# Kernel tuning notes

Hardware: AMD Instinct MI355X
Metric: run time of the kernel (lower is better)

The kernel has to match this reference:

```python
import jax, jax.numpy as jnp
import numpy as np

N_CYCLES = 20000  # number of cycles in the cycle basis (segments)


def setup_inputs() -> dict:
    key = jax.random.key(0)
    k1, k2, k3, k4, k5 = jax.random.split(key, 5)
    B, NB, E = 256, 50000, 160000  # batch, n_branches, total cycle-basis entries
    c = jax.random.normal(k1, (B, NB), dtype=jnp.float32)
    s = jax.random.normal(k2, (B, NB), dtype=jnp.float32)
    # signs are +/-1
    cysigns = jnp.where(jax.random.uniform(k4, (E,)) < 0.5, -1.0, 1.0).astype(jnp.float32)
    cyinds = jax.random.randint(k3, (E,), 0, NB, dtype=jnp.int32)
    # from_value_rowids requires nondecreasing row ids
    cyrows = jnp.sort(jax.random.randint(k5, (E,), 0, N_CYCLES, dtype=jnp.int32))
    return {"c": c, "s": s, "cysigns": cysigns, "cyinds": cyinds, "cyrows": cyrows}


def reference(c, s, cysigns, cyinds, cyrows):
    # gather branch vars per cycle-basis entry: [B, E]
    cg = jnp.take(c, cyinds, axis=1)
    sg = cysigns * jnp.take(s, cyinds, axis=1)
    # tf.math.angle(tf.complex(rc, rs)) == atan2(imag, real)
    ang = jnp.arctan2(sg, cg)  # [B, E]
    # ragged per-cycle sum == segment_sum over the entry axis -> [N_CYCLES, B]
    v_kvl = jax.ops.segment_sum(ang.T, cyrows, num_segments=N_CYCLES)
    # scalar KVL violation
    return jnp.mean(jnp.abs(v_kvl))
```

## Files before the change

kernel.cpp:

```cpp
#include <hip/hip_runtime.h>

#define NB     50000
#define NB4    12500
#define BATCH  256
#define NCYC   20000
#define QSCALE  (127.0f / 3.14159265358979f)
#define DQSCALE (3.14159265358979f / 127.0f)
#define OUTSCALE (1.0f / ((float)NCYC * (float)BATCH))

__device__ __forceinline__ float fast_atan2q(float y, float x) {
    const float ax = __builtin_fabsf(x);
    const float ay = __builtin_fabsf(y);
    const float mx = fmaxf(ax, ay);
    const float mn = fminf(ax, ay);
    const float t  = mn * __builtin_amdgcn_rcpf(mx);
    const float t2 = t * t;
    float p = fmaf(t2, fmaf(t2, fmaf(t2, fmaf(t2,
                  0.84219761f, -3.44137383f), 7.28200966f), -13.35163894f),
                  40.42416382f);
    p *= t;
    p = (ay > ax) ? (63.5f - p) : p;
    p = (x < 0.0f) ? (127.0f - p) : p;
    return copysignf(p, y);
}

__device__ __forceinline__ unsigned int q8(float y, float x) {
    return (unsigned int)(unsigned char)(signed char)__float2int_rn(fast_atan2q(y, x));
}

__device__ __forceinline__ void gload16(const void* g, void* l) {
    __builtin_amdgcn_global_load_lds(
        (const __attribute__((address_space(1))) void*)g,
        (__attribute__((address_space(3))) void*)l,
        16, 0, 0);
}

__global__ __launch_bounds__(256) void theta_k(
        const float4* __restrict__ c4, const float4* __restrict__ s4,
        signed char* __restrict__ th, int* __restrict__ row_start,
        const int* __restrict__ rows, int E) {
    __shared__ float4 ct[16][64];
    __shared__ float4 st[16][64];
    const int u = threadIdx.x;

    if (blockIdx.y == 0) {
        const int g = blockIdx.x * 256 + u;
        if (g <= NCYC) {
            int lo = 0, hi = E;
            while (lo < hi) { const int m = (lo + hi) >> 1; if (rows[m] < g) lo = m + 1; else hi = m; }
            row_start[g] = lo;
        }
    }

    const int lane  = u & 63;
    const int w     = u >> 6;
    const int brow0 = blockIdx.y * 16;
    int col = blockIdx.x * 64 + lane;
    if (col > NB4 - 1) col = NB4 - 1;

    #pragma unroll
    for (int i = 0; i < 4; ++i) {
        const int r = 4 * w + i;
        gload16(&c4[(size_t)(brow0 + r) * NB4 + col], &ct[r][0]);
        gload16(&s4[(size_t)(brow0 + r) * NB4 + col], &st[r][0]);
    }
    __syncthreads();

    const float* cf = reinterpret_cast<const float*>(ct);
    const float* sf = reinterpret_cast<const float*>(st);
    unsigned int wv[4] = {0u, 0u, 0u, 0u};
    #pragma unroll
    for (int r = 0; r < 16; ++r) {
        const float cc = cf[r * 256 + u];
        const float ss = sf[r * 256 + u];
        wv[r >> 2] |= q8(ss, cc) << (8 * (r & 3));
    }

    const int nbg = blockIdx.x * 256 + u;
    if (nbg < NB) {
        uint4 o;
        o.x = wv[0]; o.y = wv[1]; o.z = wv[2]; o.w = wv[3];
        *reinterpret_cast<uint4*>(&th[(size_t)nbg * BATCH + brow0]) = o;
    }
}

__global__ __launch_bounds__(256) void kvl3_k(
        const signed char* __restrict__ th,
        const float* __restrict__ signs, const int* __restrict__ inds,
        const int* __restrict__ row_start,
        float* __restrict__ partials) {
    __shared__ float wsum[4];
    const int tid  = threadIdx.x;
    const int wave = tid >> 6;
    const int lane = tid & 63;
    const int r    = blockIdx.x * 4 + wave;
    const int start = row_start[r];
    const int end   = row_start[r + 1];

    float a0 = 0.f, a1 = 0.f, a2 = 0.f, a3 = 0.f;
    int e = start;
    for (; e + 2 <= end; e += 2) {
        const int   i0 = inds[e],  i1 = inds[e + 1];
        const float g0 = signs[e] * DQSCALE, g1 = signs[e + 1] * DQSCALE;
        const unsigned int u0 = *reinterpret_cast<const unsigned int*>(&th[(size_t)i0 * BATCH + lane * 4]);
        const unsigned int u1 = *reinterpret_cast<const unsigned int*>(&th[(size_t)i1 * BATCH + lane * 4]);
        a0 += g0 * (float)(signed char)(u0      ) + g1 * (float)(signed char)(u1      );
        a1 += g0 * (float)(signed char)(u0 >>  8) + g1 * (float)(signed char)(u1 >>  8);
        a2 += g0 * (float)(signed char)(u0 >> 16) + g1 * (float)(signed char)(u1 >> 16);
        a3 += g0 * (float)(signed char)(u0 >> 24) + g1 * (float)(signed char)(u1 >> 24);
    }
    if (e < end) {
        const float g0 = signs[e] * DQSCALE;
        const unsigned int u0 = *reinterpret_cast<const unsigned int*>(&th[(size_t)inds[e] * BATCH + lane * 4]);
        a0 += g0 * (float)(signed char)(u0      );
        a1 += g0 * (float)(signed char)(u0 >>  8);
        a2 += g0 * (float)(signed char)(u0 >> 16);
        a3 += g0 * (float)(signed char)(u0 >> 24);
    }
    float v = fabsf(a0) + fabsf(a1) + fabsf(a2) + fabsf(a3);
    #pragma unroll
    for (int off = 32; off > 0; off >>= 1)
        v += __shfl_down(v, off, 64);
    if (lane == 0) wsum[wave] = v;
    __syncthreads();
    if (tid == 0)
        partials[blockIdx.x] = wsum[0] + wsum[1] + wsum[2] + wsum[3];
}

__global__ __launch_bounds__(1024) void reduce_k(
        const float* __restrict__ partials, float* __restrict__ out) {
    const int tid = threadIdx.x;
    float v = 0.f;
    for (int i = tid; i < NCYC / 4; i += 1024) v += partials[i];
    #pragma unroll
    for (int off = 32; off > 0; off >>= 1)
        v += __shfl_down(v, off, 64);
    __shared__ float wsum[16];
    if ((tid & 63) == 0) wsum[tid >> 6] = v;
    __syncthreads();
    if (tid == 0) {
        float t = 0.f;
        #pragma unroll
        for (int w = 0; w < 16; ++w) t += wsum[w];
        out[0] = t * OUTSCALE;
    }
}

__global__ void zero_out_k(float* out) { if (threadIdx.x == 0) out[0] = 0.0f; }

__global__ __launch_bounds__(256) void kvl_fallback_k(
        const float* __restrict__ c, const float* __restrict__ s,
        const float* __restrict__ signs, const int* __restrict__ inds,
        const int* __restrict__ rows, int E, float* __restrict__ out) {
    const int r = blockIdx.x;
    int lo = 0, hi = E;
    while (lo < hi) { const int m = (lo + hi) >> 1; if (rows[m] < r) lo = m + 1; else hi = m; }
    const int start = lo;
    hi = E;
    while (lo < hi) { const int m = (lo + hi) >> 1; if (rows[m] <= r) lo = m + 1; else hi = m; }
    const int end = lo;
    const int tid = threadIdx.x;
    float acc = 0.f;
    for (int e = start; e < end; ++e) {
        const int idx = inds[e];
        const float sg = signs[e];
        acc += atan2f(sg * s[(size_t)tid * NB + idx], c[(size_t)tid * NB + idx]);
    }
    float v = fabsf(acc);
    #pragma unroll
    for (int off = 32; off > 0; off >>= 1)
        v += __shfl_down(v, off, 64);
    __shared__ float wsum[4];
    if ((tid & 63) == 0) wsum[tid >> 6] = v;
    __syncthreads();
    if (tid == 0)
        atomicAdd(out, (wsum[0] + wsum[1] + wsum[2] + wsum[3]) *
                       (1.0f / ((float)NCYC * (float)BATCH)));
}

extern "C" void kernel_launch(void* const* d_in, const int* in_sizes, int n_in,
                              void* d_out, int out_size, void* d_ws, size_t ws_size,
                              hipStream_t stream) {
    const float* c       = (const float*)d_in[0];
    const float* s       = (const float*)d_in[1];
    const float* cysigns = (const float*)d_in[2];
    const int*   cyinds  = (const int*)d_in[3];
    const int*   cyrows  = (const int*)d_in[4];
    const int    E       = in_sizes[2];
    float* out = (float*)d_out;

    const size_t th_bytes = (size_t)NB * BATCH;
    const size_t rs_bytes = (size_t)(NCYC + 1) * sizeof(int);
    const size_t pa_bytes = (size_t)(NCYC / 4) * sizeof(float);
    const size_t need = th_bytes + rs_bytes + pa_bytes;
    if (ws_size >= need) {
        signed char* th   = (signed char*)d_ws;
        int* row_start    = (int*)(th + th_bytes);
        float* partials   = (float*)((char*)row_start + rs_bytes);

        dim3 tg((NB4 + 63) / 64, 16);
        theta_k<<<tg, 256, 0, stream>>>((const float4*)c, (const float4*)s,
                                        th, row_start, cyrows, E);
        kvl3_k<<<NCYC / 4, 256, 0, stream>>>(th, cysigns, cyinds, row_start,
                                             partials);
        reduce_k<<<1, 1024, 0, stream>>>(partials, out);
    } else {
        zero_out_k<<<1, 64, 0, stream>>>(out);
        kvl_fallback_k<<<NCYC, 256, 0, stream>>>(c, s, cysigns, cyinds, cyrows, E, out);
    }
}
```

Before: 152.7 us.

## Double-buffer per-wave theta tiles and unroll the KVL gather loop by four

theta_k now gives each wave its own 256-branch by 16-batch unit, streamed in eight two-row tiles. Async global-to-LDS loads are double-buffered with explicit vmcnt waits, so the atan2 quantization of one tile overlaps the loads of the next. This replaces the old load-all, barrier, compute pattern and its block-wide sync, and the launch becomes a flat 784-block grid. kvl3_k unrolls its entry loop from two to four to keep more random gathers in flight. The hand-written waitcnt scheme depends on exact load counts and on LDS reads finishing before a buffer is refilled.

```diff
diff --git a/kernel.cpp b/kernel.cpp
--- a/kernel.cpp
+++ b/kernel.cpp
@@ -7,6 +7,8 @@
 #define QSCALE  (127.0f / 3.14159265358979f)
 #define DQSCALE (3.14159265358979f / 127.0f)
 #define OUTSCALE (1.0f / ((float)NCYC * (float)BATCH))
+
+#define WAITV(n) asm volatile("s_waitcnt vmcnt(" #n ")" ::: "memory")
 
 __device__ __forceinline__ float fast_atan2q(float y, float x) {
     const float ax = __builtin_fabsf(x);
@@ -35,15 +37,31 @@
         16, 0, 0);
 }
 
+template<int T>
+__device__ __forceinline__ void compute_tile(
+        const float (*cbw)[2][256], const float (*sbw)[2][256],
+        int lane, unsigned int acc[4][4]) {
+    constexpr int bf = T & 1;
+    #pragma unroll
+    for (int k = 0; k < 4; ++k) {
+        const float c0 = cbw[bf][0][lane + 64 * k];
+        const float s0 = sbw[bf][0][lane + 64 * k];
+        const float c1 = cbw[bf][1][lane + 64 * k];
+        const float s1 = sbw[bf][1][lane + 64 * k];
+        acc[k][T >> 1] |= (q8(s0, c0) << (8 * ((2 * T) & 3)))
+                        | (q8(s1, c1) << (8 * ((2 * T) & 3) + 8));
+    }
+}
+
 __global__ __launch_bounds__(256) void theta_k(
         const float4* __restrict__ c4, const float4* __restrict__ s4,
         signed char* __restrict__ th, int* __restrict__ row_start,
         const int* __restrict__ rows, int E) {
-    __shared__ float4 ct[16][64];
-    __shared__ float4 st[16][64];
+    __shared__ float cb[4][2][2][256];
+    __shared__ float sb[4][2][2][256];
     const int u = threadIdx.x;
 
-    if (blockIdx.y == 0) {
+    {
         const int g = blockIdx.x * 256 + u;
         if (g <= NCYC) {
             int lo = 0, hi = E;
@@ -52,35 +70,45 @@
         }
     }
 
-    const int lane  = u & 63;
-    const int w     = u >> 6;
-    const int brow0 = blockIdx.y * 16;
-    int col = blockIdx.x * 64 + lane;
-    if (col > NB4 - 1) col = NB4 - 1;
-
-    #pragma unroll
-    for (int i = 0; i < 4; ++i) {
-        const int r = 4 * w + i;
-        gload16(&c4[(size_t)(brow0 + r) * NB4 + col], &ct[r][0]);
-        gload16(&s4[(size_t)(brow0 + r) * NB4 + col], &st[r][0]);
-    }
-    __syncthreads();
-
-    const float* cf = reinterpret_cast<const float*>(ct);
-    const float* sf = reinterpret_cast<const float*>(st);
-    unsigned int wv[4] = {0u, 0u, 0u, 0u};
-    #pragma unroll
-    for (int r = 0; r < 16; ++r) {
-        const float cc = cf[r * 256 + u];
-        const float ss = sf[r * 256 + u];
-        wv[r >> 2] |= q8(ss, cc) << (8 * (r & 3));
-    }
-
-    const int nbg = blockIdx.x * 256 + u;
-    if (nbg < NB) {
-        uint4 o;
-        o.x = wv[0]; o.y = wv[1]; o.z = wv[2]; o.w = wv[3];
-        *reinterpret_cast<uint4*>(&th[(size_t)nbg * BATCH + brow0]) = o;
+    const int lane   = u & 63;
+    const int w      = u >> 6;
+    const int unit   = blockIdx.x * 4 + w;
+    const int panel  = unit >> 4;
+    const int bchunk = unit & 15;
+    const int b0     = bchunk * 16;
+    const int nb0    = panel * 256;
+    int gcol = panel * 64 + lane;
+    if (gcol > NB4 - 1) gcol = NB4 - 1;
+
+    #define ISSUE(t) do {                                                    \
+        const int rb_ = b0 + 2 * (t);                                        \
+        gload16(&c4[(size_t)(rb_    ) * NB4 + gcol], &cb[w][(t) & 1][0][0]); \
+        gload16(&c4[(size_t)(rb_ + 1) * NB4 + gcol], &cb[w][(t) & 1][1][0]); \
+        gload16(&s4[(size_t)(rb_    ) * NB4 + gcol], &sb[w][(t) & 1][0][0]); \
+        gload16(&s4[(size_t)(rb_ + 1) * NB4 + gcol], &sb[w][(t) & 1][1][0]); \
+    } while (0)
+
+    unsigned int acc[4][4] = {{0u,0u,0u,0u},{0u,0u,0u,0u},{0u,0u,0u,0u},{0u,0u,0u,0u}};
+
+    ISSUE(0); ISSUE(1);
+    WAITV(4); compute_tile<0>(cb[w], sb[w], lane, acc); ISSUE(2);
+    WAITV(4); compute_tile<1>(cb[w], sb[w], lane, acc); ISSUE(3);
+    WAITV(4); compute_tile<2>(cb[w], sb[w], lane, acc); ISSUE(4);
+    WAITV(4); compute_tile<3>(cb[w], sb[w], lane, acc); ISSUE(5);
+    WAITV(4); compute_tile<4>(cb[w], sb[w], lane, acc); ISSUE(6);
+    WAITV(4); compute_tile<5>(cb[w], sb[w], lane, acc); ISSUE(7);
+    WAITV(4); compute_tile<6>(cb[w], sb[w], lane, acc);
+    WAITV(0); compute_tile<7>(cb[w], sb[w], lane, acc);
+    #undef ISSUE
+
+    #pragma unroll
+    for (int k = 0; k < 4; ++k) {
+        const int nb = nb0 + lane + 64 * k;
+        if (nb < NB) {
+            uint4 o;
+            o.x = acc[k][0]; o.y = acc[k][1]; o.z = acc[k][2]; o.w = acc[k][3];
+            *reinterpret_cast<uint4*>(&th[(size_t)nb * BATCH + b0]) = o;
+        }
     }
 }
 
@@ -99,17 +127,25 @@
 
     float a0 = 0.f, a1 = 0.f, a2 = 0.f, a3 = 0.f;
     int e = start;
-    for (; e + 2 <= end; e += 2) {
-        const int   i0 = inds[e],  i1 = inds[e + 1];
-        const float g0 = signs[e] * DQSCALE, g1 = signs[e + 1] * DQSCALE;
+    for (; e + 4 <= end; e += 4) {
+        const int   i0 = inds[e],     i1 = inds[e + 1];
+        const int   i2 = inds[e + 2], i3 = inds[e + 3];
+        const float g0 = signs[e]     * DQSCALE, g1 = signs[e + 1] * DQSCALE;
+        const float g2 = signs[e + 2] * DQSCALE, g3 = signs[e + 3] * DQSCALE;
         const unsigned int u0 = *reinterpret_cast<const unsigned int*>(&th[(size_t)i0 * BATCH + lane * 4]);
         const unsigned int u1 = *reinterpret_cast<const unsigned int*>(&th[(size_t)i1 * BATCH + lane * 4]);
-        a0 += g0 * (float)(signed char)(u0      ) + g1 * (float)(signed char)(u1      );
-        a1 += g0 * (float)(signed char)(u0 >>  8) + g1 * (float)(signed char)(u1 >>  8);
-        a2 += g0 * (float)(signed char)(u0 >> 16) + g1 * (float)(signed char)(u1 >> 16);
-        a3 += g0 * (float)(signed char)(u0 >> 24) + g1 * (float)(signed char)(u1 >> 24);
-    }
-    if (e < end) {
+        const unsigned int u2 = *reinterpret_cast<const unsigned int*>(&th[(size_t)i2 * BATCH + lane * 4]);
+        const unsigned int u3 = *reinterpret_cast<const unsigned int*>(&th[(size_t)i3 * BATCH + lane * 4]);
+        a0 += g0 * (float)(signed char)(u0      ) + g1 * (float)(signed char)(u1      )
+            + g2 * (float)(signed char)(u2      ) + g3 * (float)(signed char)(u3      );
+        a1 += g0 * (float)(signed char)(u0 >>  8) + g1 * (float)(signed char)(u1 >>  8)
+            + g2 * (float)(signed char)(u2 >>  8) + g3 * (float)(signed char)(u3 >>  8);
+        a2 += g0 * (float)(signed char)(u0 >> 16) + g1 * (float)(signed char)(u1 >> 16)
+            + g2 * (float)(signed char)(u2 >> 16) + g3 * (float)(signed char)(u3 >> 16);
+        a3 += g0 * (float)(signed char)(u0 >> 24) + g1 * (float)(signed char)(u1 >> 24)
+            + g2 * (float)(signed char)(u2 >> 24) + g3 * (float)(signed char)(u3 >> 24);
+    }
+    for (; e < end; ++e) {
         const float g0 = signs[e] * DQSCALE;
         const unsigned int u0 = *reinterpret_cast<const unsigned int*>(&th[(size_t)inds[e] * BATCH + lane * 4]);
         a0 += g0 * (float)(signed char)(u0      );
@@ -198,9 +234,8 @@
         int* row_start    = (int*)(th + th_bytes);
         float* partials   = (float*)((char*)row_start + rs_bytes);
 
-        dim3 tg((NB4 + 63) / 64, 16);
-        theta_k<<<tg, 256, 0, stream>>>((const float4*)c, (const float4*)s,
-                                        th, row_start, cyrows, E);
+        theta_k<<<784, 256, 0, stream>>>((const float4*)c, (const float4*)s,
+                                         th, row_start, cyrows, E);
         kvl3_k<<<NCYC / 4, 256, 0, stream>>>(th, cysigns, cyinds, row_start,
                                              partials);
         reduce_k<<<1, 1024, 0, stream>>>(partials, out);
```

After: 150.5 us. No clear change (-1.5%).
